# Performance work log

Hardware: AMD Instinct MI355X
Metric: run time of the kernel (lower is better)

The kernel has to match this reference:

```python
import jax, jax.numpy as jnp
import numpy as np

T = 2048
D_MODEL = 4096
N_HEADS = 32
N_GROUPS = 8
HEAD_DIM = 128


def _rope_tables(tokens, head_dim, base=10000.0):
    inv_freq = 1.0 / (base ** (np.arange(0, head_dim, 2, dtype=np.float32) / head_dim))
    pos = np.arange(tokens, dtype=np.float32)
    freqs = np.einsum('t,d->td', pos, inv_freq)          # [T, D/2]
    emb = np.concatenate([freqs, freqs], axis=-1)         # [T, D]
    return jnp.asarray(np.cos(emb)), jnp.asarray(np.sin(emb))


def setup_inputs() -> dict:
    key = jax.random.key(0)
    k1, k2, k3 = jax.random.split(key, 3)
    x = jax.random.normal(k1, (T, D_MODEL), dtype=jnp.float32)
    w_qkv = jax.random.normal(k2, (D_MODEL, (N_HEADS + 2 * N_GROUPS) * HEAD_DIM), dtype=jnp.float32) * 0.02
    w_out = jax.random.normal(k3, (N_HEADS * HEAD_DIM, D_MODEL), dtype=jnp.float32) * 0.02
    cos, sin = _rope_tables(T, HEAD_DIM)
    mask = jnp.tril(jnp.ones((T, T), dtype=bool))  # causal: [suffix_tokens, total_tokens]
    return {"x": x, "w_qkv": w_qkv, "w_out": w_out, "cos": cos, "sin": sin, "mask": mask}


def _rotate_half(u):
    u1, u2 = jnp.split(u, 2, axis=-1)
    return jnp.concatenate([-u2, u1], axis=-1)


def _apply_rope(u, cos, sin):
    # u: [tokens, heads, head_dim]; cos/sin: [tokens, head_dim]
    c = cos[:, None, :]
    s = sin[:, None, :]
    return u * c + _rotate_half(u) * s


def reference(x, w_qkv, w_out, cos, sin, mask):
    group_dim = N_HEADS // N_GROUPS
    qkv = x @ w_qkv                                        # [T, (H+2G)*D]
    q, k, v = jnp.split(qkv, [N_HEADS * HEAD_DIM, (N_HEADS + N_GROUPS) * HEAD_DIM], axis=-1)
    q = q.reshape(T, N_HEADS, HEAD_DIM)
    k = k.reshape(T, N_GROUPS, HEAD_DIM)
    v = v.reshape(T, N_GROUPS, HEAD_DIM)
    q = _apply_rope(q, cos, sin)
    k = _apply_rope(k, cos, sin)
    # GQA: group queries -> [T, G, group_dim, D]
    qg = q.reshape(T, N_GROUPS, group_dim, HEAD_DIM)
    scale = 1.0 / jnp.sqrt(jnp.asarray(HEAD_DIM, dtype=q.dtype))
    scores = jnp.einsum('tghd,sgd->ghts', qg, k) * scale   # [G, gd, T, S]
    neg = jnp.asarray(jnp.finfo(scores.dtype).min, scores.dtype)
    scores = jnp.where(mask[None, None, :, :], scores, neg)
    probs = jax.nn.softmax(scores, axis=-1)
    out = jnp.einsum('ghts,sgd->tghd', probs, v)           # [T, G, gd, D]
    out = out.reshape(T, N_HEADS * HEAD_DIM)
    return out @ w_out                                     # [T, model_dim]
```

## Files before the change

kernel.cpp:

```cpp
#include <hip/hip_runtime.h>
#include <cstdint>
#include <cstddef>

#define TT   2048
#define DM   4096
#define NH   32
#define NG   8
#define HD   128
#define QKVN 6144
#define KOFF 4096
#define VOFF 5120

typedef __attribute__((ext_vector_type(8))) short bf16x8;
typedef __attribute__((ext_vector_type(4))) float f32x4;
typedef unsigned short u16;

__device__ __forceinline__ u16 f2b(float f) {
  unsigned u = __builtin_bit_cast(unsigned, f);
  u += 0x7fffu + ((u >> 16) & 1u);
  return (u16)(u >> 16);
}
__device__ __forceinline__ float b2f(u16 s) {
  unsigned u = ((unsigned)s) << 16;
  return __builtin_bit_cast(float, u);
}

__device__ __forceinline__ void gload_lds16(const void* g, void* l) {
  __builtin_amdgcn_global_load_lds(
      (const __attribute__((address_space(1))) unsigned int*)g,
      (__attribute__((address_space(3))) unsigned int*)l,
      16, 0, 0);
}

__global__ __launch_bounds__(256) void cvt_f32_bf16(
    const float* __restrict__ src, u16* __restrict__ dst, int n) {
  for (int i = (blockIdx.x * 256 + threadIdx.x) * 4; i < n; i += gridDim.x * 256 * 4) {
    float4 v = *(const float4*)(src + i);
    ushort4 o;
    o.x = f2b(v.x); o.y = f2b(v.y); o.z = f2b(v.z); o.w = f2b(v.w);
    *(ushort4*)(dst + i) = o;
  }
}

__global__ __launch_bounds__(256) void transpose_cvt(
    const float* __restrict__ src, u16* __restrict__ dst, int R, int C) {
  __shared__ __align__(16) u16 tile[64 * 68];
  const int rb = blockIdx.y * 64, cb = blockIdx.x * 64;
  const int tid = threadIdx.x;
#pragma unroll
  for (int it = 0; it < 4; ++it) {
    const int idx = it * 256 + tid;
    const int r = idx >> 4, c4 = (idx & 15) * 4;
    const float4 v = *(const float4*)(src + (size_t)(rb + r) * C + cb + c4);
    tile[(c4 + 0) * 68 + r] = f2b(v.x);
    tile[(c4 + 1) * 68 + r] = f2b(v.y);
    tile[(c4 + 2) * 68 + r] = f2b(v.z);
    tile[(c4 + 3) * 68 + r] = f2b(v.w);
  }
  __syncthreads();
#pragma unroll
  for (int it = 0; it < 4; ++it) {
    const int idx = it * 256 + tid;
    const int c = idx >> 4, r4 = (idx & 15) * 4;
    const ushort4 o = *(const ushort4*)&tile[c * 68 + r4];
    *(ushort4*)(dst + (size_t)(cb + c) * R + rb + r4) = o;
  }
}

template <int WN, bool OUT_BF16>
__global__ __launch_bounds__(512) void gemm8p(
    const u16* __restrict__ A, const u16* __restrict__ Bt, void* __restrict__ Cout,
    int M, int N, int K, int nbx) {
  __shared__ __align__(16) u16 sA[2][128 * 64];
  __shared__ __align__(16) u16 sB[2][WN * 64 * 64];
  const int tid = threadIdx.x;
  const int wid = tid >> 6, lane = tid & 63;
  const int lane15 = lane & 15, laneh = lane >> 4;
  const int wm = wid >> 2, wn = wid & 3;
  const int cpx = gridDim.x >> 3;
  const int swz = ((int)blockIdx.x & 7) * cpx + ((int)blockIdx.x >> 3);
  const int m0 = (swz / nbx) * 128, n0 = (swz % nbx) * (WN * 64);
  const int xorL = (lane15 & 7) << 3;

  f32x4 acc[4][WN];
#pragma unroll
  for (int m = 0; m < 4; ++m)
#pragma unroll
    for (int n = 0; n < WN; ++n)
#pragma unroll
      for (int r = 0; r < 4; ++r) acc[m][n][r] = 0.f;

  auto stageA = [&](int buf, int t) {
    const int k0 = t << 6;
#pragma unroll
    for (int i = 0; i < 2; ++i) {
      const int ebase = (wid * 2 + i) * 512;
      const int e = ebase + lane * 8;
      const int row = e >> 6;
      const int col = (e & 63) ^ ((row & 7) << 3);
      gload_lds16(A + (size_t)(m0 + row) * K + k0 + col, &sA[buf][ebase]);
    }
  };
  auto stageB = [&](int buf, int t) {
    const int k0 = t << 6;
#pragma unroll
    for (int i = 0; i < WN; ++i) {
      const int ebase = (wid * WN + i) * 512;
      const int e = ebase + lane * 8;
      const int row = e >> 6;
      const int col = (e & 63) ^ ((row & 7) << 3);
      gload_lds16(Bt + (size_t)(n0 + row) * K + k0 + col, &sB[buf][ebase]);
    }
  };

  const int NT = K >> 6;
  stageA(0, 0);
  stageB(0, 0);
  stageA(1, 1);
  asm volatile("s_waitcnt vmcnt(2)");
  __builtin_amdgcn_s_barrier();

  for (int u = 0; u < NT; ++u) {
    const int cur = u & 1;
    bf16x8 af[4][2], bfr[WN][2];
#pragma unroll
    for (int m = 0; m < 4; ++m)
#pragma unroll
      for (int ks = 0; ks < 2; ++ks)
        af[m][ks] = *(const bf16x8*)&sA[cur][(wm * 64 + m * 16 + lane15) * 64 +
                                            ((ks * 32 + laneh * 8) ^ xorL)];
#pragma unroll
    for (int n = 0; n < WN / 2; ++n)
#pragma unroll
      for (int ks = 0; ks < 2; ++ks)
        bfr[n][ks] = *(const bf16x8*)&sB[cur][(wn * (WN * 16) + n * 16 + lane15) * 64 +
                                             ((ks * 32 + laneh * 8) ^ xorL)];
    if (u + 1 < NT) stageB(cur ^ 1, u + 1);
    __builtin_amdgcn_sched_barrier(0);
    __builtin_amdgcn_s_setprio(1);
#pragma unroll
    for (int ks = 0; ks < 2; ++ks)
#pragma unroll
      for (int m = 0; m < 4; ++m)
#pragma unroll
        for (int n = 0; n < WN / 2; ++n)
          acc[m][n] = __builtin_amdgcn_mfma_f32_16x16x32_bf16(af[m][ks], bfr[n][ks], acc[m][n], 0, 0, 0);
    __builtin_amdgcn_s_setprio(0);
    __builtin_amdgcn_s_barrier();
#pragma unroll
    for (int n = WN / 2; n < WN; ++n)
#pragma unroll
      for (int ks = 0; ks < 2; ++ks)
        bfr[n][ks] = *(const bf16x8*)&sB[cur][(wn * (WN * 16) + n * 16 + lane15) * 64 +
                                             ((ks * 32 + laneh * 8) ^ xorL)];
    if (u + 2 < NT) stageA(cur, u + 2);
    __builtin_amdgcn_sched_barrier(0);
    __builtin_amdgcn_s_setprio(1);
#pragma unroll
    for (int ks = 0; ks < 2; ++ks)
#pragma unroll
      for (int m = 0; m < 4; ++m)
#pragma unroll
        for (int n = WN / 2; n < WN; ++n)
          acc[m][n] = __builtin_amdgcn_mfma_f32_16x16x32_bf16(af[m][ks], bfr[n][ks], acc[m][n], 0, 0, 0);
    __builtin_amdgcn_s_setprio(0);
    if (u + 2 < NT) asm volatile("s_waitcnt vmcnt(2)");
    else            asm volatile("s_waitcnt vmcnt(0)");
    __builtin_amdgcn_s_barrier();
  }
#pragma unroll
  for (int m = 0; m < 4; ++m)
#pragma unroll
    for (int n = 0; n < WN; ++n)
#pragma unroll
      for (int r = 0; r < 4; ++r) {
        const int row = m0 + wm * 64 + m * 16 + laneh * 4 + r;
        const int col = n0 + wn * (WN * 16) + n * 16 + lane15;
        const float v = acc[m][n][r];
        if (OUT_BF16) ((u16*)Cout)[(size_t)row * N + col] = f2b(v);
        else          ((float*)Cout)[(size_t)row * N + col] = v;
      }
}

__global__ __launch_bounds__(256) void rope_rearrange(
    const u16* __restrict__ qkv, const float* __restrict__ cosT,
    const float* __restrict__ sinT, u16* __restrict__ Qr, u16* __restrict__ Kr) {
  const int u = blockIdx.x * 4 + (threadIdx.x >> 6);
  const int lane = threadIdx.x & 63;
  const int t = u & (TT - 1);
  const int e = u >> 11;
  const u16* in;
  u16* outp;
  if (e < NH) {
    in = qkv + (size_t)t * QKVN + e * HD;
    outp = Qr + ((size_t)e * TT + t) * HD;
  } else {
    const int g = e - NH;
    in = qkv + (size_t)t * QKVN + KOFF + g * HD;
    outp = Kr + ((size_t)g * TT + t) * HD;
  }
  const float u1 = b2f(in[lane]), u2 = b2f(in[lane + 64]);
  const float c1 = cosT[t * HD + lane], s1 = sinT[t * HD + lane];
  const float c2 = cosT[t * HD + lane + 64], s2 = sinT[t * HD + lane + 64];
  outp[lane]      = f2b(u1 * c1 - u2 * s1);
  outp[lane + 64] = f2b(u2 * c2 + u1 * s2);
}

__global__ __launch_bounds__(256) void vtrans(
    const u16* __restrict__ qkv, u16* __restrict__ VT) {
  __shared__ u16 tile[64][66];
  const int g = blockIdx.z;
  const int t0 = blockIdx.x * 64, d0 = blockIdx.y * 64;
  const int tid = threadIdx.x;
#pragma unroll
  for (int it = 0; it < 16; ++it) {
    int idx = it * 256 + tid;
    int i = idx >> 6, j = idx & 63;
    tile[i][j] = qkv[(size_t)(t0 + i) * QKVN + VOFF + g * HD + d0 + j];
  }
  __syncthreads();
#pragma unroll
  for (int it = 0; it < 16; ++it) {
    int idx = it * 256 + tid;
    int j = idx >> 6, i = idx & 63;
    VT[((size_t)g * HD + d0 + j) * TT + t0 + i] = tile[i][j];
  }
}

__global__ __launch_bounds__(512) void attn(
    const u16* __restrict__ Qr, const u16* __restrict__ Kr,
    const u16* __restrict__ VT, u16* __restrict__ AO) {
  __shared__ __align__(16) u16 sK[2][128 * 128];
  __shared__ __align__(16) u16 sV[2][128 * 128];
  __shared__ __align__(16) u16 sP[8][16 * 128];
  const int bid = blockIdx.x;
  const int swz = (bid & 7) * 32 + (bid >> 3);
  const int h = swz >> 3, p = swz & 7;
  const int g = h >> 2;
  const int tid = threadIdx.x, wid = tid >> 6, lane = tid & 63;
  const int lane15 = lane & 15, laneh = lane >> 4;
  const int xorL = (lane15 & 7) << 3;
  const u16* Qh = Qr + (size_t)h * TT * HD;
  const u16* Kg = Kr + (size_t)g * TT * HD;
  const u16* Vg = VT + (size_t)g * HD * TT;
  const float scale = 0.08838834764831845f;

  auto stageKV = [&](int buf, int kv) {
#pragma unroll
    for (int i = 0; i < 4; ++i) {
      const int ebase = (wid * 4 + i) * 512;
      const int e = ebase + lane * 8;
      const int row = e >> 7;
      const int col = (e & 127) ^ ((row & 7) << 3);
      gload_lds16(Kg + (size_t)(kv * 128 + row) * HD + col, &sK[buf][ebase]);
      gload_lds16(Vg + (size_t)row * TT + kv * 128 + col, &sV[buf][ebase]);
    }
  };

  for (int pass = 0; pass < 2; ++pass) {
    const int qt = pass ? (15 - p) : p;
    bf16x8 qf[4];
    const int qrow0 = qt * 128 + wid * 16;
#pragma unroll
    for (int ks = 0; ks < 4; ++ks)
      qf[ks] = *(const bf16x8*)(Qh + (size_t)(qrow0 + lane15) * HD + ks * 32 + laneh * 8);

    f32x4 acc_o[8];
    float mrow[4], lrow[4];
#pragma unroll
    for (int n = 0; n < 8; ++n)
#pragma unroll
      for (int r = 0; r < 4; ++r) acc_o[n][r] = 0.f;
#pragma unroll
    for (int r = 0; r < 4; ++r) { mrow[r] = -1e30f; lrow[r] = 0.f; }

    stageKV(0, 0);
    for (int kv = 0; kv <= qt; ++kv) {
      const int cur = kv & 1;
      if (kv < qt) stageKV(cur ^ 1, kv + 1);
      __builtin_amdgcn_sched_barrier(0);
      if (kv < qt) asm volatile("s_waitcnt vmcnt(8)");
      else         asm volatile("s_waitcnt vmcnt(0)");
      __builtin_amdgcn_s_barrier();

      f32x4 s[8];
#pragma unroll
      for (int n = 0; n < 8; ++n)
#pragma unroll
        for (int r = 0; r < 4; ++r) s[n][r] = 0.f;
      __builtin_amdgcn_s_setprio(1);
#pragma unroll
      for (int ks = 0; ks < 4; ++ks) {
        bf16x8 kf[8];
#pragma unroll
        for (int n = 0; n < 8; ++n)
          kf[n] = *(const bf16x8*)&sK[cur][(n * 16 + lane15) * 128 + ((ks * 32 + laneh * 8) ^ xorL)];
#pragma unroll
        for (int n = 0; n < 8; ++n)
          s[n] = __builtin_amdgcn_mfma_f32_16x16x32_bf16(qf[ks], kf[n], s[n], 0, 0, 0);
      }
      __builtin_amdgcn_s_setprio(0);

      if (kv == qt) {
#pragma unroll
        for (int n = 0; n < 8; ++n)
#pragma unroll
          for (int r = 0; r < 4; ++r) {
            const int ql = wid * 16 + laneh * 4 + r;
            const int sl = n * 16 + lane15;
            s[n][r] = (sl > ql) ? -1e30f : s[n][r] * scale;
          }
      } else {
#pragma unroll
        for (int n = 0; n < 8; ++n)
#pragma unroll
          for (int r = 0; r < 4; ++r) s[n][r] *= scale;
      }
#pragma unroll
      for (int r = 0; r < 4; ++r) {
        float pm = s[0][r];
#pragma unroll
        for (int n = 1; n < 8; ++n) pm = fmaxf(pm, s[n][r]);
        pm = fmaxf(pm, __shfl_xor(pm, 1));
        pm = fmaxf(pm, __shfl_xor(pm, 2));
        pm = fmaxf(pm, __shfl_xor(pm, 4));
        pm = fmaxf(pm, __shfl_xor(pm, 8));
        const float mnew = fmaxf(mrow[r], pm);
        const float corr = __expf(mrow[r] - mnew);
        mrow[r] = mnew;
        float ps = 0.f;
#pragma unroll
        for (int n = 0; n < 8; ++n) {
          const float pr = __expf(s[n][r] - mnew);
          s[n][r] = pr;
          ps += pr;
        }
        ps += __shfl_xor(ps, 1); ps += __shfl_xor(ps, 2);
        ps += __shfl_xor(ps, 4); ps += __shfl_xor(ps, 8);
        lrow[r] = lrow[r] * corr + ps;
#pragma unroll
        for (int n = 0; n < 8; ++n) acc_o[n][r] *= corr;
      }
#pragma unroll
      for (int n = 0; n < 8; ++n)
#pragma unroll
        for (int r = 0; r < 4; ++r) {
          const int prow = laneh * 4 + r;
          const int pcol = (n * 16 + lane15) ^ ((prow & 7) << 3);
          sP[wid][prow * 128 + pcol] = f2b(s[n][r]);
        }
      __builtin_amdgcn_s_setprio(1);
#pragma unroll
      for (int ks = 0; ks < 4; ++ks) {
        bf16x8 pf, vf[8];
        pf = *(const bf16x8*)&sP[wid][lane15 * 128 + ((ks * 32 + laneh * 8) ^ xorL)];
#pragma unroll
        for (int n = 0; n < 8; ++n)
          vf[n] = *(const bf16x8*)&sV[cur][(n * 16 + lane15) * 128 + ((ks * 32 + laneh * 8) ^ xorL)];
#pragma unroll
        for (int n = 0; n < 8; ++n)
          acc_o[n] = __builtin_amdgcn_mfma_f32_16x16x32_bf16(pf, vf[n], acc_o[n], 0, 0, 0);
      }
      __builtin_amdgcn_s_setprio(0);
      __builtin_amdgcn_s_barrier();
    }
    float inv[4];
#pragma unroll
    for (int r = 0; r < 4; ++r) inv[r] = 1.f / lrow[r];
#pragma unroll
    for (int n = 0; n < 8; ++n)
#pragma unroll
      for (int r = 0; r < 4; ++r) {
        const int trow = qt * 128 + wid * 16 + laneh * 4 + r;
        AO[(size_t)trow * DM + h * HD + n * 16 + lane15] = f2b(acc_o[n][r] * inv[r]);
      }
  }
}

extern "C" void kernel_launch(void* const* d_in, const int* in_sizes, int n_in,
                              void* d_out, int out_size, void* d_ws, size_t ws_size,
                              hipStream_t stream) {
  const float* x     = (const float*)d_in[0];
  const float* w_qkv = (const float*)d_in[1];
  const float* w_out = (const float*)d_in[2];
  const float* cosT  = (const float*)d_in[3];
  const float* sinT  = (const float*)d_in[4];
  float* out = (float*)d_out;

  char* ws = (char*)d_ws;
  u16* wT  = (u16*)(ws);
  u16* xb  = (u16*)(ws + 50331648);
  u16* qkv = (u16*)(ws + 50331648 + 16777216);
  u16* Qr  = (u16*)(ws + 50331648 + 16777216 + 25165824);
  u16* Kr  = Qr + (size_t)NH * TT * HD;
  u16* VT  = Kr + (size_t)NG * TT * HD;
  u16* AO  = xb;

  cvt_f32_bf16<<<2048, 256, 0, stream>>>(x, xb, TT * DM);
  transpose_cvt<<<dim3(QKVN / 64, DM / 64), 256, 0, stream>>>(w_qkv, wT, DM, QKVN);
  gemm8p<6, true><<<dim3((TT / 128) * (QKVN / 384)), 512, 0, stream>>>(
      xb, wT, qkv, TT, QKVN, DM, QKVN / 384);
  rope_rearrange<<<(TT * (NH + NG)) / 4, 256, 0, stream>>>(qkv, cosT, sinT, Qr, Kr);
  vtrans<<<dim3(TT / 64, HD / 64, NG), 256, 0, stream>>>(qkv, VT);
  transpose_cvt<<<dim3(DM / 64, DM / 64), 256, 0, stream>>>(w_out, wT, DM, DM);
  attn<<<NH * 8, 512, 0, stream>>>(Qr, Kr, VT, AO);
  gemm8p<4, false><<<dim3((TT / 128) * (DM / 256)), 512, 0, stream>>>(
      AO, wT, out, TT, DM, DM, DM / 256);
}
```

Baseline: 317.5 us.

## Split attention warps over query rows and key halves to raise fragment reuse

The attention kernel's wave layout changes. Each wave now covers 32 query rows and half of each 128-key tile, instead of 16 query rows and the full tile. Each K and V fragment loaded from LDS is therefore reused by two query sub-tiles, which cuts LDS read traffic per MFMA. The two key-halves keep separate online-softmax state and are merged at the end through LDS scratch that reuses the P and K buffers. The cost is more accumulator registers, extra barriers and a merge step per query tile.

```diff
diff --git a/kernel.cpp b/kernel.cpp
--- a/kernel.cpp
+++ b/kernel.cpp
@@ -232,18 +232,21 @@
     const u16* __restrict__ VT, u16* __restrict__ AO) {
   __shared__ __align__(16) u16 sK[2][128 * 128];
   __shared__ __align__(16) u16 sV[2][128 * 128];
-  __shared__ __align__(16) u16 sP[8][16 * 128];
+  __shared__ __align__(16) u16 sP[8][32 * 64];
   const int bid = blockIdx.x;
   const int swz = (bid & 7) * 32 + (bid >> 3);
   const int h = swz >> 3, p = swz & 7;
   const int g = h >> 2;
   const int tid = threadIdx.x, wid = tid >> 6, lane = tid & 63;
   const int lane15 = lane & 15, laneh = lane >> 4;
+  const int qw = wid >> 1, sw = wid & 1;
   const int xorL = (lane15 & 7) << 3;
   const u16* Qh = Qr + (size_t)h * TT * HD;
   const u16* Kg = Kr + (size_t)g * TT * HD;
   const u16* Vg = VT + (size_t)g * HD * TT;
   const float scale = 0.08838834764831845f;
+  float* mlbuf = (float*)&sP[0][0];
+  float* obuf  = (float*)&sK[0][0];
 
   auto stageKV = [&](int buf, int kv) {
 #pragma unroll
@@ -259,20 +262,25 @@
 
   for (int pass = 0; pass < 2; ++pass) {
     const int qt = pass ? (15 - p) : p;
-    bf16x8 qf[4];
-    const int qrow0 = qt * 128 + wid * 16;
-#pragma unroll
-    for (int ks = 0; ks < 4; ++ks)
-      qf[ks] = *(const bf16x8*)(Qh + (size_t)(qrow0 + lane15) * HD + ks * 32 + laneh * 8);
-
-    f32x4 acc_o[8];
-    float mrow[4], lrow[4];
-#pragma unroll
-    for (int n = 0; n < 8; ++n)
-#pragma unroll
-      for (int r = 0; r < 4; ++r) acc_o[n][r] = 0.f;
-#pragma unroll
-    for (int r = 0; r < 4; ++r) { mrow[r] = -1e30f; lrow[r] = 0.f; }
+    bf16x8 qf[2][4];
+    const int qrow0 = qt * 128 + qw * 32;
+#pragma unroll
+    for (int m = 0; m < 2; ++m)
+#pragma unroll
+      for (int ks = 0; ks < 4; ++ks)
+        qf[m][ks] = *(const bf16x8*)(Qh + (size_t)(qrow0 + m * 16 + lane15) * HD + ks * 32 + laneh * 8);
+
+    f32x4 acc[2][8];
+    float mrow[2][4], lrow[2][4];
+#pragma unroll
+    for (int m = 0; m < 2; ++m) {
+#pragma unroll
+      for (int n = 0; n < 8; ++n)
+#pragma unroll
+        for (int r = 0; r < 4; ++r) acc[m][n][r] = 0.f;
+#pragma unroll
+      for (int r = 0; r < 4; ++r) { mrow[m][r] = -1e30f; lrow[m][r] = 0.f; }
+    }
 
     stageKV(0, 0);
     for (int kv = 0; kv <= qt; ++kv) {
@@ -283,97 +291,157 @@
       else         asm volatile("s_waitcnt vmcnt(0)");
       __builtin_amdgcn_s_barrier();
 
-      f32x4 s[8];
-#pragma unroll
-      for (int n = 0; n < 8; ++n)
-#pragma unroll
-        for (int r = 0; r < 4; ++r) s[n][r] = 0.f;
+      f32x4 s[2][4];
+#pragma unroll
+      for (int m = 0; m < 2; ++m)
+#pragma unroll
+        for (int n = 0; n < 4; ++n)
+#pragma unroll
+          for (int r = 0; r < 4; ++r) s[m][n][r] = 0.f;
       __builtin_amdgcn_s_setprio(1);
 #pragma unroll
       for (int ks = 0; ks < 4; ++ks) {
-        bf16x8 kf[8];
-#pragma unroll
-        for (int n = 0; n < 8; ++n)
-          kf[n] = *(const bf16x8*)&sK[cur][(n * 16 + lane15) * 128 + ((ks * 32 + laneh * 8) ^ xorL)];
-#pragma unroll
-        for (int n = 0; n < 8; ++n)
-          s[n] = __builtin_amdgcn_mfma_f32_16x16x32_bf16(qf[ks], kf[n], s[n], 0, 0, 0);
+        bf16x8 kf[4];
+#pragma unroll
+        for (int n = 0; n < 4; ++n)
+          kf[n] = *(const bf16x8*)&sK[cur][(sw * 64 + n * 16 + lane15) * 128 +
+                                          ((ks * 32 + laneh * 8) ^ xorL)];
+#pragma unroll
+        for (int m = 0; m < 2; ++m)
+#pragma unroll
+          for (int n = 0; n < 4; ++n)
+            s[m][n] = __builtin_amdgcn_mfma_f32_16x16x32_bf16(qf[m][ks], kf[n], s[m][n], 0, 0, 0);
       }
       __builtin_amdgcn_s_setprio(0);
 
       if (kv == qt) {
 #pragma unroll
+        for (int m = 0; m < 2; ++m)
+#pragma unroll
+          for (int n = 0; n < 4; ++n)
+#pragma unroll
+            for (int r = 0; r < 4; ++r) {
+              const int ql = qw * 32 + m * 16 + laneh * 4 + r;
+              const int sl = sw * 64 + n * 16 + lane15;
+              s[m][n][r] = (sl > ql) ? -1e30f : s[m][n][r] * scale;
+            }
+      } else {
+#pragma unroll
+        for (int m = 0; m < 2; ++m)
+#pragma unroll
+          for (int n = 0; n < 4; ++n)
+#pragma unroll
+            for (int r = 0; r < 4; ++r) s[m][n][r] *= scale;
+      }
+#pragma unroll
+      for (int m = 0; m < 2; ++m)
+#pragma unroll
+        for (int r = 0; r < 4; ++r) {
+          float pm = s[m][0][r];
+#pragma unroll
+          for (int n = 1; n < 4; ++n) pm = fmaxf(pm, s[m][n][r]);
+          pm = fmaxf(pm, __shfl_xor(pm, 1));
+          pm = fmaxf(pm, __shfl_xor(pm, 2));
+          pm = fmaxf(pm, __shfl_xor(pm, 4));
+          pm = fmaxf(pm, __shfl_xor(pm, 8));
+          const float mnew = fmaxf(mrow[m][r], pm);
+          const float corr = __expf(mrow[m][r] - mnew);
+          mrow[m][r] = mnew;
+          float ps = 0.f;
+#pragma unroll
+          for (int n = 0; n < 4; ++n) {
+            const float pr = __expf(s[m][n][r] - mnew);
+            s[m][n][r] = pr;
+            ps += pr;
+          }
+          ps += __shfl_xor(ps, 1); ps += __shfl_xor(ps, 2);
+          ps += __shfl_xor(ps, 4); ps += __shfl_xor(ps, 8);
+          lrow[m][r] = lrow[m][r] * corr + ps;
+#pragma unroll
+          for (int n = 0; n < 8; ++n) acc[m][n][r] *= corr;
+        }
+#pragma unroll
+      for (int m = 0; m < 2; ++m)
+#pragma unroll
+        for (int n = 0; n < 4; ++n)
+#pragma unroll
+          for (int r = 0; r < 4; ++r) {
+            const int prow = m * 16 + laneh * 4 + r;
+            const int pcol = (n * 16 + lane15) ^ ((prow & 7) << 3);
+            sP[wid][prow * 64 + pcol] = f2b(s[m][n][r]);
+          }
+      __builtin_amdgcn_s_setprio(1);
+#pragma unroll
+      for (int ks = 0; ks < 2; ++ks) {
+        bf16x8 pf[2], vf[8];
+#pragma unroll
+        for (int m = 0; m < 2; ++m)
+          pf[m] = *(const bf16x8*)&sP[wid][(m * 16 + lane15) * 64 + ((ks * 32 + laneh * 8) ^ xorL)];
+#pragma unroll
         for (int n = 0; n < 8; ++n)
-#pragma unroll
-          for (int r = 0; r < 4; ++r) {
-            const int ql = wid * 16 + laneh * 4 + r;
-            const int sl = n * 16 + lane15;
-            s[n][r] = (sl > ql) ? -1e30f : s[n][r] * scale;
-          }
-      } else {
-#pragma unroll
-        for (int n = 0; n < 8; ++n)
-#pragma unroll
-          for (int r = 0; r < 4; ++r) s[n][r] *= scale;
-      }
-#pragma unroll
-      for (int r = 0; r < 4; ++r) {
-        float pm = s[0][r];
-#pragma unroll
-        for (int n = 1; n < 8; ++n) pm = fmaxf(pm, s[n][r]);
-        pm = fmaxf(pm, __shfl_xor(pm, 1));
-        pm = fmaxf(pm, __shfl_xor(pm, 2));
-        pm = fmaxf(pm, __shfl_xor(pm, 4));
-        pm = fmaxf(pm, __shfl_xor(pm, 8));
-        const float mnew = fmaxf(mrow[r], pm);
-        const float corr = __expf(mrow[r] - mnew);
-        mrow[r] = mnew;
-        float ps = 0.f;
-#pragma unroll
-        for (int n = 0; n < 8; ++n) {
-          const float pr = __expf(s[n][r] - mnew);
-          s[n][r] = pr;
-          ps += pr;
-        }
-        ps += __shfl_xor(ps, 1); ps += __shfl_xor(ps, 2);
-        ps += __shfl_xor(ps, 4); ps += __shfl_xor(ps, 8);
-        lrow[r] = lrow[r] * corr + ps;
-#pragma unroll
-        for (int n = 0; n < 8; ++n) acc_o[n][r] *= corr;
-      }
-#pragma unroll
-      for (int n = 0; n < 8; ++n)
-#pragma unroll
-        for (int r = 0; r < 4; ++r) {
-          const int prow = laneh * 4 + r;
-          const int pcol = (n * 16 + lane15) ^ ((prow & 7) << 3);
-          sP[wid][prow * 128 + pcol] = f2b(s[n][r]);
-        }
-      __builtin_amdgcn_s_setprio(1);
-#pragma unroll
-      for (int ks = 0; ks < 4; ++ks) {
-        bf16x8 pf, vf[8];
-        pf = *(const bf16x8*)&sP[wid][lane15 * 128 + ((ks * 32 + laneh * 8) ^ xorL)];
-#pragma unroll
-        for (int n = 0; n < 8; ++n)
-          vf[n] = *(const bf16x8*)&sV[cur][(n * 16 + lane15) * 128 + ((ks * 32 + laneh * 8) ^ xorL)];
-#pragma unroll
-        for (int n = 0; n < 8; ++n)
-          acc_o[n] = __builtin_amdgcn_mfma_f32_16x16x32_bf16(pf, vf[n], acc_o[n], 0, 0, 0);
+          vf[n] = *(const bf16x8*)&sV[cur][(n * 16 + lane15) * 128 +
+                                          ((sw * 64 + ks * 32 + laneh * 8) ^ xorL)];
+#pragma unroll
+        for (int m = 0; m < 2; ++m)
+#pragma unroll
+          for (int n = 0; n < 8; ++n)
+            acc[m][n] = __builtin_amdgcn_mfma_f32_16x16x32_bf16(pf[m], vf[n], acc[m][n], 0, 0, 0);
       }
       __builtin_amdgcn_s_setprio(0);
       __builtin_amdgcn_s_barrier();
     }
-    float inv[4];
-#pragma unroll
-    for (int r = 0; r < 4; ++r) inv[r] = 1.f / lrow[r];
-#pragma unroll
-    for (int n = 0; n < 8; ++n)
+
+    if (lane15 == 0) {
+#pragma unroll
+      for (int m = 0; m < 2; ++m)
+#pragma unroll
+        for (int r = 0; r < 4; ++r) {
+          const int row = m * 16 + laneh * 4 + r;
+          mlbuf[(qw * 2 + sw) * 32 + row] = mrow[m][r];
+          mlbuf[256 + (qw * 2 + sw) * 32 + row] = lrow[m][r];
+        }
+    }
+    __builtin_amdgcn_s_barrier();
+    float sc[2][4], Lr[2][4];
+#pragma unroll
+    for (int m = 0; m < 2; ++m)
 #pragma unroll
       for (int r = 0; r < 4; ++r) {
-        const int trow = qt * 128 + wid * 16 + laneh * 4 + r;
-        AO[(size_t)trow * DM + h * HD + n * 16 + lane15] = f2b(acc_o[n][r] * inv[r]);
+        const int row = m * 16 + laneh * 4 + r;
+        const float mp = mlbuf[(qw * 2 + (sw ^ 1)) * 32 + row];
+        const float lp = mlbuf[256 + (qw * 2 + (sw ^ 1)) * 32 + row];
+        const float M = fmaxf(mrow[m][r], mp);
+        sc[m][r] = __expf(mrow[m][r] - M);
+        Lr[m][r] = lrow[m][r] * sc[m][r] + lp * __expf(mp - M);
       }
+    if (sw == 0) {
+#pragma unroll
+      for (int m = 0; m < 2; ++m)
+#pragma unroll
+        for (int n = 0; n < 8; ++n)
+#pragma unroll
+          for (int r = 0; r < 4; ++r) {
+            const int row = m * 16 + laneh * 4 + r;
+            const int col = (n * 16 + lane15) ^ ((row & 7) << 3);
+            obuf[qw * 4096 + row * 128 + col] = acc[m][n][r] * sc[m][r];
+          }
+    }
+    __builtin_amdgcn_s_barrier();
+    if (sw == 1) {
+#pragma unroll
+      for (int m = 0; m < 2; ++m)
+#pragma unroll
+        for (int n = 0; n < 8; ++n)
+#pragma unroll
+          for (int r = 0; r < 4; ++r) {
+            const int row = m * 16 + laneh * 4 + r;
+            const int col = (n * 16 + lane15) ^ ((row & 7) << 3);
+            const float o = obuf[qw * 4096 + row * 128 + col] + acc[m][n][r] * sc[m][r];
+            const int trow = qt * 128 + qw * 32 + row;
+            AO[(size_t)trow * DM + h * HD + n * 16 + lane15] = f2b(o / Lr[m][r]);
+          }
+    }
+    __builtin_amdgcn_s_barrier();
   }
 }
 
```

Measured after the change: 385.9 us. +21.6%, slower.
